# Performance work log

Hardware: AMD Instinct MI355X
Metric: run time of the kernel (lower is better)

## Reference

```python
import jax, jax.numpy as jnp
import numpy as np
from jax.scipy.special import logsumexp

NUM_WAY = 64
NUM_SHOT = 5
NUM_QUERY = 195
FEAT_DIM = 1536
LAM = 10.0
ALPHA = 0.2
N_EPOCHS = 20
N_LAB = NUM_WAY * NUM_SHOT          # labeled samples
EPS = 1e-6
MAXITERS = 1000


def setup_inputs() -> dict:
    key = jax.random.key(0)
    n = NUM_WAY * (NUM_SHOT + NUM_QUERY)
    # non-negative features (module applies sqrt power-transform)
    X = jax.random.uniform(key, (n, FEAT_DIM), dtype=jnp.float32)
    # ordering (shot/query-major, way-minor) required by init_from_labelled's reshape
    labels = (jnp.arange(n) % NUM_WAY).astype(jnp.int32)
    return {"X": X, "labels": labels}


def _l2norm(x):
    return x / jnp.clip(jnp.linalg.norm(x, axis=-1, keepdims=True), 1e-12, None)


def _cdist(a, b):
    d2 = jnp.sum(a * a, 1)[:, None] + jnp.sum(b * b, 1)[None, :] - 2.0 * (a @ b.T)
    return jnp.sqrt(jnp.maximum(d2, 0.0))


def _log_sinkhorn(M):
    """Log-domain Sinkhorn on cost M with row marginal 1 and column marginal NUM_QUERY.
    Mirrors GaussianModel.compute_optimal_transport (P=exp(-lam*M); P/=P.sum(); alternate
    row/col rescale until row-sum change <= eps or maxiters), returned in log space."""
    logP0 = -LAM * M
    logP0 = logP0 - logsumexp(logP0)          # P /= P.sum()
    n, m = M.shape
    log_r = jnp.zeros((n,), M.dtype)          # r = ones
    log_c = jnp.full((m,), jnp.log(jnp.float32(NUM_QUERY)), M.dtype)  # c = num_query each

    def cond(state):
        f, g, u_prev, it = state
        rows = jnp.exp(logsumexp(logP0 + f[:, None] + g[None, :], axis=1))
        return (jnp.max(jnp.abs(u_prev - rows)) > EPS) & (it < MAXITERS)

    def body(state):
        f, g, u_prev, it = state
        lr = logsumexp(logP0 + f[:, None] + g[None, :], axis=1)
        f = f + log_r - lr                    # row rescale: P *= (r/u)
        lc = logsumexp(logP0 + f[:, None] + g[None, :], axis=0)
        g = g + log_c - lc                    # col rescale: P *= (c/colsum)
        return (f, g, jnp.exp(lr), it + 1)

    z = jnp.zeros((n,), M.dtype)
    f, g, _, _ = jax.lax.while_loop(cond, body, (z, jnp.zeros((m,), M.dtype), z, 0))
    return logP0 + f[:, None] + g[None, :]


def _get_probas(Z, mus, labels):
    dist = _cdist(Z, mus)                      # [n, way]
    logP_test = _log_sinkhorn(dist[N_LAB:])    # [n_us, way] (log plan)
    onehot = jax.nn.one_hot(labels[:N_LAB], NUM_WAY, dtype=Z.dtype)  # labeled rows: hard 0/1
    return jnp.concatenate([onehot, logP_test], axis=0)


def reference(X, labels):
    X = jnp.sqrt(X + 1e-6)                     # power transform
    X = _l2norm(X)
    Xl = X[:N_LAB] - X[:N_LAB].mean(0, keepdims=True)
    Xu = X[N_LAB:] - X[N_LAB:].mean(0, keepdims=True)
    Z = _l2norm(jnp.concatenate([Xl, Xu], axis=0))
    # init mus from labeled shots: (shot+query, way, d)[:shot].mean(0)
    mus = Z.reshape(NUM_SHOT + NUM_QUERY, NUM_WAY, -1)[:NUM_SHOT].mean(0)
    for _ in range(N_EPOCHS):                  # EM loop
        p_xj = _get_probas(Z, mus, labels)
        mask = jnp.exp(p_xj)                   # NB: labeled rows become {1, e} as in original
        emus = (mask.T @ Z) / mask.sum(0)[:, None]
        mus = mus + ALPHA * (emus - mus)
    P = _get_probas(Z, mus, labels)
    y_hat = jnp.argmax(P, axis=-1)
    matches = (labels == y_hat).astype(jnp.float32)
    acc = matches[N_LAB:].mean()
    pm = jnp.std(acc) * 1.96                   # std of scalar (unbiased=False) -> 0
    return (P, acc, pm)
```

## Files before the change

### kernel.cpp

```cpp
#include <hip/hip_runtime.h>
#include <math.h>

#define NW 64
#define NS 5
#define NQ 195
#define DIM 1536
#define NTOT 12800
#define NL 320
#define NU 12480
#define NUP 12544
#define ALPHA 0.2f
#define EPOCHS 20
#define EPSC 1e-6f
#define MAXIT 1000
#define SB_NB 49
#define NSLAB 7

typedef float f32x4 __attribute__((ext_vector_type(4)));
typedef short short8 __attribute__((ext_vector_type(8)));

__device__ inline float wave_sum(float x){
#pragma unroll
  for(int o=32;o;o>>=1) x += __shfl_xor(x,o);
  return x;
}
__device__ inline float bf2f(ushort h){
  union{uint u; float f;} c; c.u = ((uint)h)<<16; return c.f;
}
__device__ inline ushort f2bf(float x){
  union{float f; uint u;} c; c.f = x;
  uint r = c.u + 0x7FFFu + ((c.u>>16)&1u);
  return (ushort)(r>>16);
}
__device__ inline void gld16(const ushort* g, ushort* l){
  __builtin_amdgcn_global_load_lds((const __attribute__((address_space(1))) void*)g,
                                   (__attribute__((address_space(3))) void*)l, 16, 0, 0);
}

__global__ __launch_bounds__(256) void k_prep(const float* __restrict__ X, ushort* __restrict__ Zhi){
  int row = blockIdx.x*4 + (threadIdx.x>>6);
  int lane = threadIdx.x & 63;
  const float4* xp = (const float4*)(X + (size_t)row*DIM);
  float4 v[6]; float ss = 0.f;
#pragma unroll
  for(int q=0;q<6;q++){
    float4 t = xp[lane + 64*q];
    t.x = sqrtf(t.x+1e-6f); t.y = sqrtf(t.y+1e-6f); t.z = sqrtf(t.z+1e-6f); t.w = sqrtf(t.w+1e-6f);
    v[q]=t; ss += t.x*t.x+t.y*t.y+t.z*t.z+t.w*t.w;
  }
  ss = wave_sum(ss);
  float inv = 1.f / fmaxf(sqrtf(ss), 1e-12f);
#pragma unroll
  for(int q=0;q<6;q++){
    float4 t = v[q];
    ushort4 h;
    h.x=f2bf(t.x*inv); h.y=f2bf(t.y*inv); h.z=f2bf(t.z*inv); h.w=f2bf(t.w*inv);
    *(ushort4*)&Zhi[(size_t)row*DIM + 4*lane + 256*q] = h;
  }
}

__global__ __launch_bounds__(256) void k_colsum(const ushort* __restrict__ Zhi,
                                                float* __restrict__ csum_l, float* __restrict__ csum_u){
  int c0 = blockIdx.x*512 + 2*threadIdx.x;
  int r0 = blockIdx.y*128;
  float al0=0.f, al1=0.f, au0=0.f, au1=0.f;
  for(int r=r0; r<r0+128; r++){
    ushort2 h = *(const ushort2*)&Zhi[(size_t)r*DIM + c0];
    float x0 = bf2f(h.x), x1 = bf2f(h.y);
    if(r < NL){ al0+=x0; al1+=x1; } else { au0+=x0; au1+=x1; }
  }
  if(r0 < NL){ atomicAdd(&csum_l[c0], al0); atomicAdd(&csum_l[c0+1], al1); }
  if(r0+128 > NL){ atomicAdd(&csum_u[c0], au0); atomicAdd(&csum_u[c0+1], au1); }
}

__global__ void k_finalize_means(float* csum_l, float* csum_u){
  int idx = blockIdx.x*256 + threadIdx.x;
  if(idx < DIM) csum_l[idx] *= (1.0f/NL);
  else if(idx < 2*DIM) csum_u[idx-DIM] *= (1.0f/NU);
}

__global__ __launch_bounds__(256) void k_center(ushort* __restrict__ Zhi,
                                                const float* __restrict__ cm_l, const float* __restrict__ cm_u){
  int row = blockIdx.x*4 + (threadIdx.x>>6);
  int lane = threadIdx.x & 63;
  const float4* cp = (const float4*)((row < NL) ? cm_l : cm_u);
  float4 v[6]; float ss = 0.f;
#pragma unroll
  for(int q=0;q<6;q++){
    ushort4 h = *(const ushort4*)&Zhi[(size_t)row*DIM + 4*lane + 256*q];
    float4 m = cp[lane + 64*q];
    float4 t;
    t.x = bf2f(h.x) - m.x; t.y = bf2f(h.y) - m.y;
    t.z = bf2f(h.z) - m.z; t.w = bf2f(h.w) - m.w;
    v[q]=t; ss += t.x*t.x+t.y*t.y+t.z*t.z+t.w*t.w;
  }
  ss = wave_sum(ss);
  float inv = 1.f / fmaxf(sqrtf(ss), 1e-12f);
#pragma unroll
  for(int q=0;q<6;q++){
    float4 t = v[q];
    ushort4 h;
    h.x=f2bf(t.x*inv); h.y=f2bf(t.y*inv); h.z=f2bf(t.z*inv); h.w=f2bf(t.w*inv);
    *(ushort4*)&Zhi[(size_t)row*DIM + 4*lane + 256*q] = h;
  }
}

__global__ __launch_bounds__(256) void k_ztrans(const ushort* __restrict__ Zhi, ushort* __restrict__ ZT){
  __shared__ ushort T[64][66];
  int ti = blockIdx.x, tc = blockIdx.y;
  int t = threadIdx.x;
  int r = t>>2, ch = (t&3)*16;
  const ushort* src = Zhi + (size_t)(NL + ti*64 + r)*DIM + tc*64 + ch;
  short8 a = *(const short8*)src;
  short8 b = *(const short8*)(src+8);
#pragma unroll
  for(int k=0;k<8;k++){ T[r][ch+k] = (ushort)a[k]; T[r][ch+8+k] = (ushort)b[k]; }
  __syncthreads();
  short8 o0, o1;
#pragma unroll
  for(int k=0;k<8;k++){ o0[k] = (short)T[ch+k][r]; o1[k] = (short)T[ch+8+k][r]; }
  ushort* dst = ZT + (size_t)(tc*64 + r)*NUP + ti*64 + ch;
  *(short8*)dst = o0;
  *(short8*)(dst+8) = o1;
}

__global__ void k_ztpad(ushort* __restrict__ ZT){
  int idx = blockIdx.x*256 + threadIdx.x;
  int c = idx >> 6, j = idx & 63;
  if(c < DIM) ZT[(size_t)c*NUP + NU + j] = 0;
}

__global__ void k_mus_init(const ushort* __restrict__ Zhi, float* __restrict__ mus){
  int w = blockIdx.x;
#pragma unroll
  for(int q=0;q<6;q++){
    int c = threadIdx.x + 256*q;
    float s = 0.f;
#pragma unroll
    for(int sh=0; sh<NS; sh++) s += bf2f(Zhi[(size_t)(sh*NW + w)*DIM + c]);
    mus[(size_t)w*DIM + c] = s * 0.2f;
  }
}

__global__ void k_vinit(float* __restrict__ vprev){
  if(threadIdx.x < 64) vprev[threadIdx.x] = 1.0f;
}

__global__ void k_slc(const float* __restrict__ mus, float* __restrict__ S){
  int c = blockIdx.x*256 + threadIdx.x;
  float s = 0.f;
  for(int w=0;w<64;w++) s += mus[(size_t)w*DIM + c];
  S[c] = 5.0f * s;
}

__global__ void k_elab(const float* __restrict__ mus, const float* __restrict__ S,
                       float* __restrict__ emus_lab){
  int idx = blockIdx.x*256 + threadIdx.x;
  int c = idx % DIM;
  emus_lab[idx] = S[c] + (expf(1.0f)-1.0f)*5.0f*mus[idx];
}

__global__ void k_epoch_prep(const float* __restrict__ mus, float* munorm, float* masksum,
                             int* stamps, ushort* __restrict__ mbh, ushort* __restrict__ mbl){
  int w = blockIdx.x;
  float ss = 0.f;
#pragma unroll
  for(int q=0;q<6;q++){
    int c = threadIdx.x + 256*q;
    float v = mus[(size_t)w*DIM + c];
    ss += v*v;
    ushort h = f2bf(v);
    mbh[(size_t)w*DIM + c] = h;
    mbl[(size_t)w*DIM + c] = f2bf(v - bf2f(h));
  }
  __shared__ float red[4];
  float wsu = wave_sum(ss);
  if((threadIdx.x&63)==0) red[threadIdx.x>>6]=wsu;
  __syncthreads();
  if(threadIdx.x==0){
    munorm[w] = red[0]+red[1]+red[2]+red[3];
    masksum[w] = 315.0f + 5.0f*expf(1.0f);
    if(w < SB_NB) stamps[w] = 0;
  }
}

__device__ inline void k_dist_stage(ushort* sm, int buf, int k0,
                                    const ushort* Zb, const ushort* mbh, const ushort* mbl,
                                    int w, int rr, int c8){
  int base = buf*12288;
#pragma unroll
  for(int j=0;j<6;j++){
    int s = 4*j + w;
    int row = (s&7)*8 + rr;
    int off = k0 + ((c8 ^ (row&7))<<3);
    const ushort* src; int dst;
    if(s < 8){        src = Zb  + (size_t)row*DIM + off; dst = base + s*512; }
    else if(s < 16){  src = mbh + (size_t)row*DIM + off; dst = base + 4096 + (s-8)*512; }
    else {            src = mbl + (size_t)row*DIM + off; dst = base + 8192 + (s-16)*512; }
    gld16(src, sm + dst);
  }
}

__global__ __launch_bounds__(256,1) void k_dist(const ushort* __restrict__ mbh, const ushort* __restrict__ mbl,
                                                const ushort* __restrict__ Zhi, const float* __restrict__ munorm,
                                                ushort* __restrict__ Kbf){
  __shared__ __align__(16) ushort sm[49152];
  int t = threadIdx.x;
  int w = t>>6, lane = t&63;
  int l15 = lane&15, q = lane>>4;
  int rr = lane>>3, c8 = lane&7;
  int e7 = l15&7;
  int b = blockIdx.x;
  const ushort* Zb = Zhi + (size_t)(NL + b*64)*DIM;
  float mn = munorm[16*w + l15];
  f32x4 acc[4];
#pragma unroll
  for(int mt=0;mt<4;mt++) acc[mt] = (f32x4){0.f,0.f,0.f,0.f};

  k_dist_stage(sm, 0, 0,   Zb, mbh, mbl, w, rr, c8);
  k_dist_stage(sm, 1, 64,  Zb, mbh, mbl, w, rr, c8);
  k_dist_stage(sm, 2, 128, Zb, mbh, mbl, w, rr, c8);

  int brow = 16*w + l15;
  for(int c=0;c<24;c++){
    if(c < 22)      asm volatile("s_waitcnt vmcnt(12)" ::: "memory");
    else if(c==22)  asm volatile("s_waitcnt vmcnt(6)"  ::: "memory");
    else            asm volatile("s_waitcnt vmcnt(0)"  ::: "memory");
    __builtin_amdgcn_sched_barrier(0);
    __builtin_amdgcn_s_barrier();
    __builtin_amdgcn_sched_barrier(0);
    if(c+3 < 24)
      k_dist_stage(sm, (c+3)&3, (c+3)*64, Zb, mbh, mbl, w, rr, c8);
    const ushort* tb = sm + (c&3)*12288;
#pragma unroll
    for(int kt=0;kt<2;kt++){
      int sw = ((kt*4 + q) ^ e7)<<3;
      short8 bh = *(const short8*)&tb[4096 + brow*64 + sw];
      short8 bl = *(const short8*)&tb[8192 + brow*64 + sw];
#pragma unroll
      for(int mt=0;mt<4;mt++){
        short8 a = *(const short8*)&tb[(mt*16 + l15)*64 + sw];
        acc[mt] = __builtin_amdgcn_mfma_f32_16x16x32_bf16(a, bh, acc[mt], 0,0,0);
        acc[mt] = __builtin_amdgcn_mfma_f32_16x16x32_bf16(a, bl, acc[mt], 0,0,0);
      }
    }
  }

#pragma unroll
  for(int mt=0;mt<4;mt++)
#pragma unroll
    for(int r=0;r<4;r++){
      float d2 = 1.0f + mn - 2.0f*acc[mt][r];
      Kbf[(size_t)(b*64 + mt*16 + q*4 + r)*NW + 16*w + l15] =
        f2bf(expf(-10.0f * sqrtf(fmaxf(d2, 0.0f))));
    }
}

__global__ __launch_bounds__(256,1) void k_sinkhorn(const ushort* __restrict__ Kbf,
                                                    ushort* __restrict__ MThi,
                                                    float* __restrict__ partials, int* __restrict__ stamps,
                                                    float* __restrict__ vprev, float* __restrict__ masksum){
  __shared__ __align__(16) float vsh[64];
  __shared__ float tmat[256][33];
  __shared__ float tq[8][64];
  __shared__ float tcol[64];
  __shared__ float mred[4];
  __shared__ float ctrl[1];
  int t = threadIdx.x, b = blockIdx.x;
  int iu = b*256 + t;
  bool active = iu < NU;
  float kr[64];
  if(active){
    const ushort* kp = Kbf + (size_t)iu*NW;
#pragma unroll
    for(int q=0;q<8;q++){
      short8 hh = *(const short8*)(kp + 8*q);
#pragma unroll
      for(int i=0;i<8;i++) kr[8*q+i] = bf2f((ushort)hh[i]);
    }
  } else {
#pragma unroll
    for(int j=0;j<64;j++) kr[j]=0.f;
  }
  if(t < 64) vsh[t] = vprev[t];
  float u = 1.0f, r_old = 0.0f;
  __syncthreads();
  int n = 0;
  while(true){
    double s = 0.0;
#pragma unroll
    for(int q=0;q<16;q++){
      float4 vv = *(const float4*)&vsh[4*q];
      s += (double)kr[4*q]*vv.x + (double)kr[4*q+1]*vv.y + (double)kr[4*q+2]*vv.z + (double)kr[4*q+3]*vv.w;
    }
    float sf = (float)s;
    float r = u * sf;
    float diff = fabsf(r - r_old);
    float u_new = (active && sf > 0.f) ? 1.0f/sf : 0.0f;
    {
      float wmx = diff;
#pragma unroll
      for(int o=32;o;o>>=1) wmx = fmaxf(wmx, __shfl_xor(wmx,o));
      if((t&63)==0) mred[t>>6] = wmx;
    }
#pragma unroll
    for(int h=0;h<2;h++){
#pragma unroll
      for(int jj=0;jj<32;jj++) tmat[t][jj] = kr[32*h+jj]*u_new;
      __syncthreads();
      {
        int j = t & 31, q = t >> 5;
        float ps = 0.f;
#pragma unroll
        for(int rr=0;rr<32;rr++) ps += tmat[q*32+rr][j];
        tq[q][j] = ps;
      }
      __syncthreads();
      if(t < 32) tcol[32*h + t] = tq[0][t]+tq[1][t]+tq[2][t]+tq[3][t]+tq[4][t]+tq[5][t]+tq[6][t]+tq[7][t];
      __syncthreads();
    }
    int buf = n & 1;
    float* P = partials + buf*(SB_NB*66) + b*66;
    if(t < 64){
      __hip_atomic_store(&P[t], tcol[t], __ATOMIC_RELAXED, __HIP_MEMORY_SCOPE_AGENT);
    } else if(t == 64){
      float bm = fmaxf(fmaxf(mred[0],mred[1]), fmaxf(mred[2],mred[3]));
      __hip_atomic_store(&P[64], bm, __ATOMIC_RELAXED, __HIP_MEMORY_SCOPE_AGENT);
    }
    __syncthreads();
    if(t == 0){
      __threadfence();
      __hip_atomic_store(&stamps[b], n+1, __ATOMIC_RELEASE, __HIP_MEMORY_SCOPE_AGENT);
    }
    if(t < SB_NB){
      while(__hip_atomic_load(&stamps[t], __ATOMIC_ACQUIRE, __HIP_MEMORY_SCOPE_AGENT) <= n){}
    }
    __syncthreads();
    {
      int j = t & 63, q4 = t >> 6;
      float ps = 0.f, pm = 0.f;
      const float* PB = partials + buf*(SB_NB*66);
#pragma unroll
      for(int i=0;i<12;i++){
        int bb = q4 + 4*i;
        ps += PB[bb*66 + j];
        pm = fmaxf(pm, PB[bb*66 + 64]);
      }
      if(q4 == 0){
        ps += PB[48*66 + j];
        pm = fmaxf(pm, PB[48*66 + 64]);
      }
      tq[q4][j] = ps;
      if(j==0) mred[q4] = pm;
    }
    __syncthreads();
    if(t==0) ctrl[0] = fmaxf(fmaxf(mred[0],mred[1]), fmaxf(mred[2],mred[3]));
    __syncthreads();
    float M = ctrl[0];
    if(M <= EPSC || n >= MAXIT) break;
    u = u_new; r_old = r; n++;
    if(t < 64) vsh[t] = (float)NQ / (tq[0][t]+tq[1][t]+tq[2][t]+tq[3][t]);
    __syncthreads();
  }
#pragma unroll
  for(int h=0;h<2;h++){
#pragma unroll
    for(int jj=0;jj<32;jj++) tmat[t][jj] = kr[32*h+jj]*u;
    __syncthreads();
    {
      int j = t & 31, q = t >> 5;
      float ps = 0.f;
#pragma unroll
      for(int rr=0;rr<32;rr++) ps += tmat[q*32+rr][j];
      tq[q][j] = ps;
    }
    __syncthreads();
    if(t < 32) tcol[32*h + t] = tq[0][t]+tq[1][t]+tq[2][t]+tq[3][t]+tq[4][t]+tq[5][t]+tq[6][t]+tq[7][t];
    __syncthreads();
  }
  if(t < 64) atomicAdd(&masksum[t], tcol[t]*vsh[t]);
  if(active){
#pragma unroll
    for(int j=0;j<64;j++)
      MThi[(size_t)j*NUP + iu] = f2bf(kr[j]*u*vsh[j]);
  } else {
#pragma unroll
    for(int j=0;j<64;j++)
      MThi[(size_t)j*NUP + iu] = 0;
  }
  if(b==0 && t<64) vprev[t] = vsh[t];
}

__device__ inline void k_emus_stage(ushort* sm, int buf, int k0,
                                    const ushort* Ab, const ushort* Bb,
                                    int w, int rr, int c8){
  int base = buf*8192;
#pragma unroll
  for(int j=0;j<4;j++){
    int s = 4*j + w;
    int row = (s&7)*8 + rr;
    int off = k0 + ((c8 ^ (row&7))<<3);
    const ushort* src; int dst;
    if(s < 8){ src = Ab + (size_t)row*NUP + off; dst = base + s*512; }
    else     { src = Bb + (size_t)row*NUP + off; dst = base + 4096 + (s-8)*512; }
    gld16(src, sm + dst);
  }
}

__global__ __launch_bounds__(256,1) void k_emus(const ushort* __restrict__ MThi, const ushort* __restrict__ ZThi,
                                                float* __restrict__ part){
  __shared__ __align__(16) ushort sm[32768];
  int t = threadIdx.x;
  int w = t>>6, lane = t&63;
  int l15 = lane&15, q = lane>>4;
  int rr = lane>>3, c8 = lane&7;
  int e7 = l15&7;
  int cx = blockIdx.x, iy = blockIdx.y;
  const ushort* Ab = MThi + iy*1792;
  const ushort* Bb = ZThi + (size_t)(cx*64)*NUP + iy*1792;
  f32x4 acc[4];
#pragma unroll
  for(int mt=0;mt<4;mt++) acc[mt] = (f32x4){0.f,0.f,0.f,0.f};

  k_emus_stage(sm, 0, 0,   Ab, Bb, w, rr, c8);
  k_emus_stage(sm, 1, 64,  Ab, Bb, w, rr, c8);
  k_emus_stage(sm, 2, 128, Ab, Bb, w, rr, c8);

  int brow = 16*w + l15;
  for(int c=0;c<28;c++){
    if(c < 26)      asm volatile("s_waitcnt vmcnt(8)" ::: "memory");
    else if(c==26)  asm volatile("s_waitcnt vmcnt(4)" ::: "memory");
    else            asm volatile("s_waitcnt vmcnt(0)" ::: "memory");
    __builtin_amdgcn_sched_barrier(0);
    __builtin_amdgcn_s_barrier();
    __builtin_amdgcn_sched_barrier(0);
    if(c+3 < 28)
      k_emus_stage(sm, (c+3)&3, (c+3)*64, Ab, Bb, w, rr, c8);
    const ushort* tb = sm + (c&3)*8192;
#pragma unroll
    for(int kt=0;kt<2;kt++){
      int sw = ((kt*4 + q) ^ e7)<<3;
      short8 bf = *(const short8*)&tb[4096 + brow*64 + sw];
#pragma unroll
      for(int mt=0;mt<4;mt++){
        short8 a = *(const short8*)&tb[(mt*16 + l15)*64 + sw];
        acc[mt] = __builtin_amdgcn_mfma_f32_16x16x32_bf16(a, bf, acc[mt], 0,0,0);
      }
    }
  }

  float* dst = part + (size_t)iy*(NW*DIM);
#pragma unroll
  for(int mt=0;mt<4;mt++)
#pragma unroll
    for(int r=0;r<4;r++)
      dst[(size_t)(mt*16 + q*4 + r)*DIM + cx*64 + 16*w + l15] = acc[mt][r];
}

__global__ void k_mus_step(float* __restrict__ mus, const float* __restrict__ emus_lab,
                           const float* __restrict__ part, float* munorm, float* masksum,
                           int* stamps, ushort* __restrict__ mbh, ushort* __restrict__ mbl){
  int w = blockIdx.x;
  float msum = masksum[w];
  float ss = 0.f;
#pragma unroll
  for(int q=0;q<6;q++){
    int c = threadIdx.x + 256*q;
    size_t idx = (size_t)w*DIM + c;
    float e = emus_lab[idx];
#pragma unroll
    for(int s=0;s<NSLAB;s++) e += part[(size_t)s*(NW*DIM) + idx];
    float nm = mus[idx] + ALPHA*(e/msum - mus[idx]);
    mus[idx] = nm;
    ss += nm*nm;
    ushort h = f2bf(nm);
    mbh[idx] = h;
    mbl[idx] = f2bf(nm - bf2f(h));
  }
  __shared__ float red[4];
  float wsu = wave_sum(ss);
  if((threadIdx.x&63)==0) red[threadIdx.x>>6]=wsu;
  __syncthreads();
  if(threadIdx.x==0){
    munorm[w] = red[0]+red[1]+red[2]+red[3];
    masksum[w] = 315.0f + 5.0f*expf(1.0f);
    if(w < SB_NB) stamps[w] = 0;
  }
}

__global__ void k_out_lab(const int* __restrict__ labels, float* __restrict__ out){
  int idx = blockIdx.x*256 + threadIdx.x;
  if(idx < NL*NW){
    int i = idx >> 6, w = idx & 63;
    out[idx] = (labels[i]==w) ? 1.0f : 0.0f;
  }
}

__global__ __launch_bounds__(256) void k_out_u(const ushort* __restrict__ MThi, float* __restrict__ out){
  __shared__ float P[64][68];
  int b = blockIdx.x;
  int iu0 = b*64;
  int t = threadIdx.x;
  int w = t>>2, ch = (t&3)*16;
  const ushort* ph = MThi + (size_t)w*NUP + iu0 + ch;
  short8 h0 = *(const short8*)ph, h1 = *(const short8*)(ph+8);
#pragma unroll
  for(int k=0;k<8;k++){
    P[ch+k][w]   = logf(bf2f((ushort)h0[k]));
    P[ch+8+k][w] = logf(bf2f((ushort)h1[k]));
  }
  __syncthreads();
  int r = t>>2, c0 = (t&3)*16;
  float4* dst = (float4*)(out + (size_t)(NL + iu0 + r)*NW + c0);
#pragma unroll
  for(int g=0;g<4;g++) dst[g] = *(float4*)&P[r][c0+4*g];
}

__global__ void k_acc(const ushort* __restrict__ MThi, const int* __restrict__ labels, float* matchcount){
  int iu = blockIdx.x*256 + threadIdx.x;
  float m = 0.f;
  if(iu < NU){
    float best = -1.f; int bj = 0;
#pragma unroll 8
    for(int w=0;w<64;w++){
      float v = bf2f(MThi[(size_t)w*NUP + iu]);
      if(v > best){ best = v; bj = w; }
    }
    m = (labels[NL+iu] == bj) ? 1.f : 0.f;
  }
  float ws = wave_sum(m);
  __shared__ float red[4];
  if((threadIdx.x&63)==0) red[threadIdx.x>>6]=ws;
  __syncthreads();
  if(threadIdx.x==0) atomicAdd(matchcount, red[0]+red[1]+red[2]+red[3]);
}

__global__ void k_fin(const float* matchcount, float* __restrict__ out){
  out[(size_t)NTOT*NW]     = (*matchcount) * (1.0f/(float)NU);
  out[(size_t)NTOT*NW + 1] = 0.0f;
}

extern "C" void kernel_launch(void* const* d_in, const int* in_sizes, int n_in,
                              void* d_out, int out_size, void* d_ws, size_t ws_size,
                              hipStream_t stream){
  const float* X = (const float*)d_in[0];
  const int* labels = (const int*)d_in[1];
  float* out = (float*)d_out;
  float* ws = (float*)d_ws;

  float*  matchcount = ws + 0;
  float*  munorm     = ws + 4;
  float*  masksum    = ws + 68;
  float*  vprev      = ws + 132;
  float*  csum_l     = ws + 196;
  float*  csum_u     = ws + 1732;
  int*    stamps     = (int*)(ws + 3268);
  float*  partials   = ws + 3332;
  float*  Slc        = ws + 9800;
  float*  mus        = ws + 11336;
  float*  emus_lab   = ws + 109640;
  ushort* mbh        = (ushort*)(ws + 207944);
  ushort* mbl        = (ushort*)(ws + 257096);
  float*  U          = ws + 306248;
  ushort* Kbf        = (ushort*)U;
  float*  part       = U;
  ushort* MThi       = (ushort*)(ws + 1092680);
  ushort* Zhi        = (ushort*)(ws + 1293384);
  ushort* ZThi       = (ushort*)(ws + 11123784);
  if(ws_size < (size_t)20757576*4) return;

  hipMemsetAsync(ws, 0, 3332*sizeof(float), stream);

  k_prep<<<3200,256,0,stream>>>(X, Zhi);
  k_colsum<<<dim3(3,100),256,0,stream>>>(Zhi, csum_l, csum_u);
  k_finalize_means<<<12,256,0,stream>>>(csum_l, csum_u);
  k_center<<<3200,256,0,stream>>>(Zhi, csum_l, csum_u);
  k_ztrans<<<dim3(195,24),256,0,stream>>>(Zhi, ZThi);
  k_ztpad<<<384,256,0,stream>>>(ZThi);
  k_mus_init<<<64,256,0,stream>>>(Zhi, mus);
  k_vinit<<<1,64,0,stream>>>(vprev);
  k_slc<<<6,256,0,stream>>>(mus, Slc);
  k_elab<<<384,256,0,stream>>>(mus, Slc, emus_lab);
  k_epoch_prep<<<64,256,0,stream>>>(mus, munorm, masksum, stamps, mbh, mbl);

  for(int e=0; e<=EPOCHS; e++){
    k_dist<<<195,256,0,stream>>>(mbh, mbl, Zhi, munorm, Kbf);
    k_sinkhorn<<<SB_NB,256,0,stream>>>(Kbf, MThi, partials, stamps, vprev, masksum);
    if(e < EPOCHS){
      k_emus<<<dim3(24,NSLAB),256,0,stream>>>(MThi, ZThi, part);
      k_mus_step<<<64,256,0,stream>>>(mus, emus_lab, part, munorm, masksum, stamps, mbh, mbl);
    }
  }
  k_out_lab<<<80,256,0,stream>>>(labels, out);
  k_out_u<<<195,256,0,stream>>>(MThi, out);
  k_acc<<<49,256,0,stream>>>(MThi, labels, matchcount);
  k_fin<<<1,1,0,stream>>>(matchcount, out);
}
```

Baseline: 1.460 ms.

## Split distance GEMM over K with atomic accumulation and fuse kernel exp into Sinkhorn

The distance kernel is split four ways along the feature dimension and accumulates raw dot products into an fp32 buffer with atomics, so the grid quadruples and occupancy rises. The sqrt/exp kernel transform moves into the Sinkhorn load, which also zeroes the buffer for reuse. The emus slab partials likewise become atomic accumulation, and the mus step reads and clears them. This trades more global atomic traffic and fp32 reads for better CU utilisation in the distance step.

```diff
diff --git a/kernel.cpp b/kernel.cpp
--- a/kernel.cpp
+++ b/kernel.cpp
@@ -201,37 +201,32 @@
   }
 }
 
-__global__ __launch_bounds__(256,1) void k_dist(const ushort* __restrict__ mbh, const ushort* __restrict__ mbl,
-                                                const ushort* __restrict__ Zhi, const float* __restrict__ munorm,
-                                                ushort* __restrict__ Kbf){
-  __shared__ __align__(16) ushort sm[49152];
+__global__ __launch_bounds__(256,3) void k_dist(const ushort* __restrict__ mbh, const ushort* __restrict__ mbl,
+                                                const ushort* __restrict__ Zhi, float* __restrict__ S){
+  __shared__ __align__(16) ushort sm[24576];
   int t = threadIdx.x;
   int w = t>>6, lane = t&63;
   int l15 = lane&15, q = lane>>4;
   int rr = lane>>3, c8 = lane&7;
   int e7 = l15&7;
-  int b = blockIdx.x;
+  int b = blockIdx.x, ks = blockIdx.y;
   const ushort* Zb = Zhi + (size_t)(NL + b*64)*DIM;
-  float mn = munorm[16*w + l15];
   f32x4 acc[4];
 #pragma unroll
   for(int mt=0;mt<4;mt++) acc[mt] = (f32x4){0.f,0.f,0.f,0.f};
 
-  k_dist_stage(sm, 0, 0,   Zb, mbh, mbl, w, rr, c8);
-  k_dist_stage(sm, 1, 64,  Zb, mbh, mbl, w, rr, c8);
-  k_dist_stage(sm, 2, 128, Zb, mbh, mbl, w, rr, c8);
+  int k0 = ks*384;
+  k_dist_stage(sm, 0, k0,      Zb, mbh, mbl, w, rr, c8);
+  k_dist_stage(sm, 1, k0+64,   Zb, mbh, mbl, w, rr, c8);
 
   int brow = 16*w + l15;
-  for(int c=0;c<24;c++){
-    if(c < 22)      asm volatile("s_waitcnt vmcnt(12)" ::: "memory");
-    else if(c==22)  asm volatile("s_waitcnt vmcnt(6)"  ::: "memory");
-    else            asm volatile("s_waitcnt vmcnt(0)"  ::: "memory");
+  for(int c=0;c<6;c++){
+    if(c < 5) asm volatile("s_waitcnt vmcnt(6)" ::: "memory");
+    else      asm volatile("s_waitcnt vmcnt(0)" ::: "memory");
     __builtin_amdgcn_sched_barrier(0);
     __builtin_amdgcn_s_barrier();
     __builtin_amdgcn_sched_barrier(0);
-    if(c+3 < 24)
-      k_dist_stage(sm, (c+3)&3, (c+3)*64, Zb, mbh, mbl, w, rr, c8);
-    const ushort* tb = sm + (c&3)*12288;
+    const ushort* tb = sm + (c&1)*12288;
 #pragma unroll
     for(int kt=0;kt<2;kt++){
       int sw = ((kt*4 + q) ^ e7)<<3;
@@ -244,23 +239,26 @@
         acc[mt] = __builtin_amdgcn_mfma_f32_16x16x32_bf16(a, bl, acc[mt], 0,0,0);
       }
     }
+    if(c+2 < 6){
+      __builtin_amdgcn_s_barrier();
+      k_dist_stage(sm, c&1, k0 + (c+2)*64, Zb, mbh, mbl, w, rr, c8);
+    }
   }
 
 #pragma unroll
   for(int mt=0;mt<4;mt++)
 #pragma unroll
-    for(int r=0;r<4;r++){
-      float d2 = 1.0f + mn - 2.0f*acc[mt][r];
-      Kbf[(size_t)(b*64 + mt*16 + q*4 + r)*NW + 16*w + l15] =
-        f2bf(expf(-10.0f * sqrtf(fmaxf(d2, 0.0f))));
-    }
-}
-
-__global__ __launch_bounds__(256,1) void k_sinkhorn(const ushort* __restrict__ Kbf,
+    for(int r=0;r<4;r++)
+      atomicAdd(&S[(size_t)(b*64 + mt*16 + q*4 + r)*NW + 16*w + l15], acc[mt][r]);
+}
+
+__global__ __launch_bounds__(256,1) void k_sinkhorn(float* __restrict__ S,
                                                     ushort* __restrict__ MThi,
                                                     float* __restrict__ partials, int* __restrict__ stamps,
-                                                    float* __restrict__ vprev, float* __restrict__ masksum){
+                                                    float* __restrict__ vprev, float* __restrict__ masksum,
+                                                    const float* __restrict__ munorm){
   __shared__ __align__(16) float vsh[64];
+  __shared__ float mnsh[64];
   __shared__ float tmat[256][33];
   __shared__ float tq[8][64];
   __shared__ float tcol[64];
@@ -269,22 +267,27 @@
   int t = threadIdx.x, b = blockIdx.x;
   int iu = b*256 + t;
   bool active = iu < NU;
+  if(t < 64){ vsh[t] = vprev[t]; mnsh[t] = munorm[t]; }
+  __syncthreads();
   float kr[64];
   if(active){
-    const ushort* kp = Kbf + (size_t)iu*NW;
-#pragma unroll
-    for(int q=0;q<8;q++){
-      short8 hh = *(const short8*)(kp + 8*q);
-#pragma unroll
-      for(int i=0;i<8;i++) kr[8*q+i] = bf2f((ushort)hh[i]);
-    }
+    float* sp = S + (size_t)iu*NW;
+#pragma unroll
+    for(int q=0;q<16;q++){
+      float4 sv = *(const float4*)(sp + 4*q);
+      kr[4*q+0] = expf(-10.0f*sqrtf(fmaxf(1.0f + mnsh[4*q+0] - 2.0f*sv.x, 0.0f)));
+      kr[4*q+1] = expf(-10.0f*sqrtf(fmaxf(1.0f + mnsh[4*q+1] - 2.0f*sv.y, 0.0f)));
+      kr[4*q+2] = expf(-10.0f*sqrtf(fmaxf(1.0f + mnsh[4*q+2] - 2.0f*sv.z, 0.0f)));
+      kr[4*q+3] = expf(-10.0f*sqrtf(fmaxf(1.0f + mnsh[4*q+3] - 2.0f*sv.w, 0.0f)));
+    }
+    float4 z4 = (float4){0.f,0.f,0.f,0.f};
+#pragma unroll
+    for(int q=0;q<16;q++) *(float4*)(sp + 4*q) = z4;
   } else {
 #pragma unroll
     for(int j=0;j<64;j++) kr[j]=0.f;
   }
-  if(t < 64) vsh[t] = vprev[t];
   float u = 1.0f, r_old = 0.0f;
-  __syncthreads();
   int n = 0;
   while(true){
     double s = 0.0;
@@ -408,7 +411,7 @@
 }
 
 __global__ __launch_bounds__(256,1) void k_emus(const ushort* __restrict__ MThi, const ushort* __restrict__ ZThi,
-                                                float* __restrict__ part){
+                                                float* __restrict__ emus){
   __shared__ __align__(16) ushort sm[32768];
   int t = threadIdx.x;
   int w = t>>6, lane = t&63;
@@ -449,16 +452,15 @@
     }
   }
 
-  float* dst = part + (size_t)iy*(NW*DIM);
 #pragma unroll
   for(int mt=0;mt<4;mt++)
 #pragma unroll
     for(int r=0;r<4;r++)
-      dst[(size_t)(mt*16 + q*4 + r)*DIM + cx*64 + 16*w + l15] = acc[mt][r];
+      atomicAdd(&emus[(size_t)(mt*16 + q*4 + r)*DIM + cx*64 + 16*w + l15], acc[mt][r]);
 }
 
 __global__ void k_mus_step(float* __restrict__ mus, const float* __restrict__ emus_lab,
-                           const float* __restrict__ part, float* munorm, float* masksum,
+                           float* __restrict__ emus, float* munorm, float* masksum,
                            int* stamps, ushort* __restrict__ mbh, ushort* __restrict__ mbl){
   int w = blockIdx.x;
   float msum = masksum[w];
@@ -467,9 +469,8 @@
   for(int q=0;q<6;q++){
     int c = threadIdx.x + 256*q;
     size_t idx = (size_t)w*DIM + c;
-    float e = emus_lab[idx];
-#pragma unroll
-    for(int s=0;s<NSLAB;s++) e += part[(size_t)s*(NW*DIM) + idx];
+    float e = emus_lab[idx] + emus[idx];
+    emus[idx] = 0.f;
     float nm = mus[idx] + ALPHA*(e/msum - mus[idx]);
     mus[idx] = nm;
     ss += nm*nm;
@@ -562,14 +563,15 @@
   ushort* mbh        = (ushort*)(ws + 207944);
   ushort* mbl        = (ushort*)(ws + 257096);
   float*  U          = ws + 306248;
-  ushort* Kbf        = (ushort*)U;
-  float*  part       = U;
-  ushort* MThi       = (ushort*)(ws + 1092680);
-  ushort* Zhi        = (ushort*)(ws + 1293384);
-  ushort* ZThi       = (ushort*)(ws + 11123784);
-  if(ws_size < (size_t)20757576*4) return;
+  float*  S          = U;
+  float*  emus       = U;
+  ushort* MThi       = (ushort*)(ws + 1104968);
+  ushort* Zhi        = (ushort*)(ws + 1305672);
+  ushort* ZThi       = (ushort*)(ws + 11136072);
+  if(ws_size < (size_t)20769864*4) return;
 
   hipMemsetAsync(ws, 0, 3332*sizeof(float), stream);
+  hipMemsetAsync(U, 0, (size_t)798720*sizeof(float), stream);
 
   k_prep<<<3200,256,0,stream>>>(X, Zhi);
   k_colsum<<<dim3(3,100),256,0,stream>>>(Zhi, csum_l, csum_u);
@@ -584,11 +586,11 @@
   k_epoch_prep<<<64,256,0,stream>>>(mus, munorm, masksum, stamps, mbh, mbl);
 
   for(int e=0; e<=EPOCHS; e++){
-    k_dist<<<195,256,0,stream>>>(mbh, mbl, Zhi, munorm, Kbf);
-    k_sinkhorn<<<SB_NB,256,0,stream>>>(Kbf, MThi, partials, stamps, vprev, masksum);
+    k_dist<<<dim3(195,4),256,0,stream>>>(mbh, mbl, Zhi, S);
+    k_sinkhorn<<<SB_NB,256,0,stream>>>(S, MThi, partials, stamps, vprev, masksum, munorm);
     if(e < EPOCHS){
-      k_emus<<<dim3(24,NSLAB),256,0,stream>>>(MThi, ZThi, part);
-      k_mus_step<<<64,256,0,stream>>>(mus, emus_lab, part, munorm, masksum, stamps, mbh, mbl);
+      k_emus<<<dim3(24,NSLAB),256,0,stream>>>(MThi, ZThi, emus);
+      k_mus_step<<<64,256,0,stream>>>(mus, emus_lab, emus, munorm, masksum, stamps, mbh, mbl);
     }
   }
   k_out_lab<<<80,256,0,stream>>>(labels, out);
```

New measurement: 1.938 ms. 32.7% more time.
